# Optimization experiments

Hardware: AMD Instinct MI355X
Metric: run time of the kernel (lower is better)

Reference implementation:

```python
import jax, jax.numpy as jnp
import numpy as np


def setup_inputs() -> dict:
    key = jax.random.key(0)
    k1, k2 = jax.random.split(key)
    N, resolution = 32, 512
    cam2world_matrix = jax.random.normal(k1, (N, 4, 4), dtype=jnp.float32)
    # keep fx, fy (divisors) away from zero
    intrinsics = jax.random.uniform(k2, (N, 3, 3), dtype=jnp.float32, minval=0.5, maxval=1.5)
    return {"cam2world_matrix": cam2world_matrix, "intrinsics": intrinsics, "resolution": resolution}


def reference(cam2world_matrix, intrinsics, resolution):
    # patch_scale=1, masked_sampling=0 default path: full_resolution == resolution
    N = cam2world_matrix.shape[0]
    M = resolution * resolution
    cam_locs_world = cam2world_matrix[:, :3, 3]              # (N, 3)
    fx = intrinsics[:, 0, 0][:, None]
    fy = intrinsics[:, 1, 1][:, None]
    cx = intrinsics[:, 0, 2][:, None]
    cy = intrinsics[:, 1, 2][:, None]
    sk = intrinsics[:, 0, 1][:, None]

    # pixel-center uv grid in [0,1); torch builds (i,j) then flips channels,
    # so x_cam is the flattened column (j) grid, y_cam the row (i) grid.
    coords = (jnp.arange(resolution, dtype=jnp.float32) + 0.5) / resolution
    ii, jj = jnp.meshgrid(coords, coords, indexing='ij')      # (R, R) each
    x_cam = jj.reshape(1, M)                                  # broadcast over N
    y_cam = ii.reshape(1, M)
    z_cam = -1.0                                              # z_cam = -ones

    x_lift = -(x_cam - cx + cy * sk / fy - sk * y_cam / fy) / fx * z_cam  # (N, M)
    y_lift = (y_cam - cy) / fy * z_cam                                    # (N, M)

    ones = jnp.ones((N, M), dtype=cam2world_matrix.dtype)
    cam_rel_points = jnp.stack(
        (jnp.broadcast_to(x_lift, (N, M)),
         jnp.broadcast_to(y_lift, (N, M)),
         -ones, ones), axis=-1)                               # (N, M, 4)

    world_rel_points = jnp.einsum('nij,nmj->nmi', cam2world_matrix, cam_rel_points)[:, :, :3]
    ray_dirs = world_rel_points - cam_locs_world[:, None, :]
    norm = jnp.maximum(jnp.linalg.norm(ray_dirs, axis=2, keepdims=True), 1e-12)
    ray_dirs = ray_dirs / norm
    ray_origins = jnp.broadcast_to(cam_locs_world[:, None, :], ray_dirs.shape)
    return ray_origins, ray_dirs
```

## Files before the change

### kernel.cpp

```cpp
#include <hip/hip_runtime.h>
#include <math.h>

typedef float f32x4 __attribute__((ext_vector_type(4)));

__global__ __launch_bounds__(256) void ray_sampler_deep(
    const float* __restrict__ c2w,
    const float* __restrict__ intr,
    float* __restrict__ out,
    int blocks_per_cam,
    int resShift,
    float inv_res,
    size_t dir_off)
{
    const unsigned n   = (unsigned)blockIdx.x / (unsigned)blocks_per_cam;
    const unsigned blk = (unsigned)blockIdx.x - n * (unsigned)blocks_per_cam;
    const unsigned f4_per_cam = (unsigned)blocks_per_cam * 2048u;

    const float* C = c2w + n * 16;
    const float* K = intr + n * 9;

    const float r00 = C[0], r01 = C[1], r02 = C[2], ox = C[3];
    const float r10 = C[4], r11 = C[5], r12 = C[6], oy = C[7];
    const float r20 = C[8], r21 = C[9], r22 = C[10], oz = C[11];
    const float fx = K[0], sk = K[1], cx = K[2];
    const float fy = K[4], cy = K[5];

    const float inv_fx = 1.0f / fx;
    const float inv_fy = 1.0f / fy;
    const unsigned rmask = (1u << resShift) - 1u;

    const unsigned q0  = blk * 2048u + threadIdx.x;
    const unsigned f00 = q0 * 4u;
    const size_t   t0  = (size_t)n * f4_per_cam + q0;

    f32x4* o4 = reinterpret_cast<f32x4*>(out);
    f32x4* d4 = reinterpret_cast<f32x4*>(out + dir_off);

    #pragma unroll
    for (int k = 0; k < 8; ++k) {
        const unsigned f0 = f00 + 1024u * (unsigned)k;
        const unsigned p0 = f0 / 3u;
        const unsigned ph = f0 - p0 * 3u;
        const float ax = (ph == 0u) ? ox : ((ph == 1u) ? oy : oz);
        const float ay = (ph == 0u) ? oy : ((ph == 1u) ? oz : ox);
        const float az = (ph == 0u) ? oz : ((ph == 1u) ? ox : oy);
        const f32x4 vo = {ax, ay, az, ax};
        o4[t0 + 256u * (unsigned)k] = vo;
    }

    #pragma unroll
    for (int k = 0; k < 8; ++k) {
        const unsigned f0 = f00 + 1024u * (unsigned)k;
        const unsigned p0 = f0 / 3u;
        const unsigned ph = f0 - p0 * 3u;

        float d0x, d0y, d0z, d1x, d1y, d1z;
        #pragma unroll
        for (int s = 0; s < 2; ++s) {
            const unsigned p = p0 + (unsigned)s;
            const unsigned i = p >> resShift;
            const unsigned j = p & rmask;

            const float y_cam  = ((float)i + 0.5f) * inv_res;
            const float ycc    = (y_cam - cy) * inv_fy;
            const float y_lift = -ycc;
            const float xc_off = -cx - sk * ycc;
            const float x_cam  = ((float)j + 0.5f) * inv_res;
            const float x_lift = (x_cam + xc_off) * inv_fx;

            const float ux = fmaf(r00, x_lift, fmaf(r01, y_lift, -r02));
            const float uy = fmaf(r10, x_lift, fmaf(r11, y_lift, -r12));
            const float uz = fmaf(r20, x_lift, fmaf(r21, y_lift, -r22));
            const float ss  = fmaf(ux, ux, fmaf(uy, uy, uz * uz));
            const float inv = rsqrtf(fmaxf(ss, 1e-24f));

            if (s == 0) { d0x = ux * inv; d0y = uy * inv; d0z = uz * inv; }
            else        { d1x = ux * inv; d1y = uy * inv; d1z = uz * inv; }
        }

        f32x4 vd;
        vd.x = (ph == 0u) ? d0x : ((ph == 1u) ? d0y : d0z);
        vd.y = (ph == 0u) ? d0y : ((ph == 1u) ? d0z : d1x);
        vd.z = (ph == 0u) ? d0z : ((ph == 1u) ? d1x : d1y);
        vd.w = (ph == 0u) ? d1x : ((ph == 1u) ? d1y : d1z);
        d4[t0 + 256u * (unsigned)k] = vd;
    }
}

extern "C" void kernel_launch(void* const* d_in, const int* in_sizes, int n_in,
                              void* d_out, int out_size, void* d_ws, size_t ws_size,
                              hipStream_t stream) {
    const float* c2w  = (const float*)d_in[0];
    const float* intr = (const float*)d_in[1];
    float* out = (float*)d_out;

    const int N = in_sizes[0] / 16;
    const long long M = (long long)out_size / (6LL * (long long)N);
    const int res = (int)(sqrt((double)M) + 0.5);

    int resShift = 0; while ((1 << resShift) < res) ++resShift;

    const long long F    = (long long)N * M * 3LL;
    const int f4_per_cam = (int)(M * 3LL / 4LL);
    const int blocks_per_cam = f4_per_cam / 2048;
    const int grid = N * blocks_per_cam;
    const size_t dir_off = (size_t)F;

    ray_sampler_deep<<<grid, 256, 0, stream>>>(c2w, intr, out,
                                               blocks_per_cam, resShift,
                                               1.0f / (float)res, dir_off);
}
```

Before: 196.1 us.

## Replace per-camera block grid with persistent grid-stride sweep and shared camera table

Swaps the fixed per-camera grid, where each thread wrote eight origin and eight direction vectors, for a persistent 1024-block grid-stride loop over the origin and direction outputs in sequence. All camera matrices and inverted intrinsics are preloaded into shared memory once per block. A specialised template path replaces the per-element camera division with a shift and divide by three when the resolution is 512. The aim is to cut launch and tail overhead and keep the write stream continuous. The cost is a per-iteration branch, index arithmetic, and fewer writes in flight per thread.

```diff
diff --git a/kernel.cpp b/kernel.cpp
--- a/kernel.cpp
+++ b/kernel.cpp
@@ -3,87 +3,94 @@
 
 typedef float f32x4 __attribute__((ext_vector_type(4)));
 
-__global__ __launch_bounds__(256) void ray_sampler_deep(
+template <bool FAST3>
+__global__ __launch_bounds__(256) void ray_sweep(
     const float* __restrict__ c2w,
     const float* __restrict__ intr,
     float* __restrict__ out,
-    int blocks_per_cam,
+    unsigned f4_per_cam,
+    unsigned F4,
+    unsigned iters,
+    int N,
     int resShift,
     float inv_res,
     size_t dir_off)
 {
-    const unsigned n   = (unsigned)blockIdx.x / (unsigned)blocks_per_cam;
-    const unsigned blk = (unsigned)blockIdx.x - n * (unsigned)blocks_per_cam;
-    const unsigned f4_per_cam = (unsigned)blocks_per_cam * 2048u;
+    extern __shared__ float cam[];
 
-    const float* C = c2w + n * 16;
-    const float* K = intr + n * 9;
+    for (int c = threadIdx.x; c < N; c += 256) {
+        const float* C = c2w + c * 16;
+        const float* K = intr + c * 9;
+        float* s = cam + c * 17;
+        s[0]=C[0]; s[1]=C[1]; s[2]=C[2];  s[3]=C[3];
+        s[4]=C[4]; s[5]=C[5]; s[6]=C[6];  s[7]=C[7];
+        s[8]=C[8]; s[9]=C[9]; s[10]=C[10]; s[11]=C[11];
+        s[12] = 1.0f / K[0];
+        s[13] = K[1];
+        s[14] = K[2];
+        s[15] = 1.0f / K[4];
+        s[16] = K[5];
+    }
+    __syncthreads();
 
-    const float r00 = C[0], r01 = C[1], r02 = C[2], ox = C[3];
-    const float r10 = C[4], r11 = C[5], r12 = C[6], oy = C[7];
-    const float r20 = C[8], r21 = C[9], r22 = C[10], oz = C[11];
-    const float fx = K[0], sk = K[1], cx = K[2];
-    const float fy = K[4], cy = K[5];
-
-    const float inv_fx = 1.0f / fx;
-    const float inv_fy = 1.0f / fy;
+    const unsigned gstride = gridDim.x * 256u;
+    unsigned g = blockIdx.x * 256u + threadIdx.x;
+    f32x4* o4 = reinterpret_cast<f32x4*>(out);
+    f32x4* d4 = reinterpret_cast<f32x4*>(out + dir_off);
     const unsigned rmask = (1u << resShift) - 1u;
 
-    const unsigned q0  = blk * 2048u + threadIdx.x;
-    const unsigned f00 = q0 * 4u;
-    const size_t   t0  = (size_t)n * f4_per_cam + q0;
-
-    f32x4* o4 = reinterpret_cast<f32x4*>(out);
-    f32x4* d4 = reinterpret_cast<f32x4*>(out + dir_off);
-
-    #pragma unroll
-    for (int k = 0; k < 8; ++k) {
-        const unsigned f0 = f00 + 1024u * (unsigned)k;
+    for (unsigned it = 0; it < iters; ++it, g += gstride) {
+        const bool isO = g < F4;
+        const unsigned q = isO ? g : g - F4;
+        const unsigned n = FAST3 ? ((q >> 16) / 3u)
+                                 : (q / f4_per_cam);
+        const unsigned r = q - n * f4_per_cam;
+        const unsigned f0 = r * 4u;
         const unsigned p0 = f0 / 3u;
         const unsigned ph = f0 - p0 * 3u;
-        const float ax = (ph == 0u) ? ox : ((ph == 1u) ? oy : oz);
-        const float ay = (ph == 0u) ? oy : ((ph == 1u) ? oz : ox);
-        const float az = (ph == 0u) ? oz : ((ph == 1u) ? ox : oy);
-        const f32x4 vo = {ax, ay, az, ax};
-        o4[t0 + 256u * (unsigned)k] = vo;
-    }
+        const float* s = cam + n * 17;
 
-    #pragma unroll
-    for (int k = 0; k < 8; ++k) {
-        const unsigned f0 = f00 + 1024u * (unsigned)k;
-        const unsigned p0 = f0 / 3u;
-        const unsigned ph = f0 - p0 * 3u;
+        if (isO) {
+            const float ox = s[3], oy = s[7], oz = s[11];
+            const float ax = (ph == 0u) ? ox : ((ph == 1u) ? oy : oz);
+            const float ay = (ph == 0u) ? oy : ((ph == 1u) ? oz : ox);
+            const float az = (ph == 0u) ? oz : ((ph == 1u) ? ox : oy);
+            const f32x4 vo = {ax, ay, az, ax};
+            o4[g] = vo;
+        } else {
+            const float r00 = s[0], r01 = s[1], r02 = s[2];
+            const float r10 = s[4], r11 = s[5], r12 = s[6];
+            const float r20 = s[8], r21 = s[9], r22 = s[10];
+            const float inv_fx = s[12], sk = s[13], cx = s[14];
+            const float inv_fy = s[15], cy = s[16];
 
-        float d0x, d0y, d0z, d1x, d1y, d1z;
-        #pragma unroll
-        for (int s = 0; s < 2; ++s) {
-            const unsigned p = p0 + (unsigned)s;
-            const unsigned i = p >> resShift;
-            const unsigned j = p & rmask;
-
-            const float y_cam  = ((float)i + 0.5f) * inv_res;
-            const float ycc    = (y_cam - cy) * inv_fy;
-            const float y_lift = -ycc;
-            const float xc_off = -cx - sk * ycc;
-            const float x_cam  = ((float)j + 0.5f) * inv_res;
-            const float x_lift = (x_cam + xc_off) * inv_fx;
-
-            const float ux = fmaf(r00, x_lift, fmaf(r01, y_lift, -r02));
-            const float uy = fmaf(r10, x_lift, fmaf(r11, y_lift, -r12));
-            const float uz = fmaf(r20, x_lift, fmaf(r21, y_lift, -r22));
-            const float ss  = fmaf(ux, ux, fmaf(uy, uy, uz * uz));
-            const float inv = rsqrtf(fmaxf(ss, 1e-24f));
-
-            if (s == 0) { d0x = ux * inv; d0y = uy * inv; d0z = uz * inv; }
-            else        { d1x = ux * inv; d1y = uy * inv; d1z = uz * inv; }
+            float d0x, d0y, d0z, d1x, d1y, d1z;
+            #pragma unroll
+            for (int st = 0; st < 2; ++st) {
+                const unsigned p = p0 + (unsigned)st;
+                const unsigned i = p >> resShift;
+                const unsigned j = p & rmask;
+                const float y_cam  = ((float)i + 0.5f) * inv_res;
+                const float ycc    = (y_cam - cy) * inv_fy;
+                const float y_lift = -ycc;
+                const float xc_off = -cx - sk * ycc;
+                const float x_cam  = ((float)j + 0.5f) * inv_res;
+                const float x_lift = (x_cam + xc_off) * inv_fx;
+                const float ux = fmaf(r00, x_lift, fmaf(r01, y_lift, -r02));
+                const float uy = fmaf(r10, x_lift, fmaf(r11, y_lift, -r12));
+                const float uz = fmaf(r20, x_lift, fmaf(r21, y_lift, -r22));
+                const float ss  = fmaf(ux, ux, fmaf(uy, uy, uz * uz));
+                const float inv = rsqrtf(fmaxf(ss, 1e-24f));
+                if (st == 0) { d0x = ux*inv; d0y = uy*inv; d0z = uz*inv; }
+                else         { d1x = ux*inv; d1y = uy*inv; d1z = uz*inv; }
+            }
+            f32x4 vd;
+            vd.x = (ph == 0u) ? d0x : ((ph == 1u) ? d0y : d0z);
+            vd.y = (ph == 0u) ? d0y : ((ph == 1u) ? d0z : d1x);
+            vd.z = (ph == 0u) ? d0z : ((ph == 1u) ? d1x : d1y);
+            vd.w = (ph == 0u) ? d1x : ((ph == 1u) ? d1y : d1z);
+            d4[q] = vd;
         }
-
-        f32x4 vd;
-        vd.x = (ph == 0u) ? d0x : ((ph == 1u) ? d0y : d0z);
-        vd.y = (ph == 0u) ? d0y : ((ph == 1u) ? d0z : d1x);
-        vd.z = (ph == 0u) ? d0z : ((ph == 1u) ? d1x : d1y);
-        vd.w = (ph == 0u) ? d1x : ((ph == 1u) ? d1y : d1z);
-        d4[t0 + 256u * (unsigned)k] = vd;
     }
 }
 
@@ -100,13 +107,24 @@
 
     int resShift = 0; while ((1 << resShift) < res) ++resShift;
 
-    const long long F    = (long long)N * M * 3LL;
-    const int f4_per_cam = (int)(M * 3LL / 4LL);
-    const int blocks_per_cam = f4_per_cam / 2048;
-    const int grid = N * blocks_per_cam;
-    const size_t dir_off = (size_t)F;
+    const long long F     = (long long)N * M * 3LL;
+    const unsigned f4pc   = (unsigned)(M * 3LL / 4LL);
+    const unsigned F4     = (unsigned)N * f4pc;
+    const size_t  dir_off = (size_t)F;
 
-    ray_sampler_deep<<<grid, 256, 0, stream>>>(c2w, intr, out,
-                                               blocks_per_cam, resShift,
-                                               1.0f / (float)res, dir_off);
+    unsigned grid = 1024;
+    while ((2ull * F4) % ((unsigned long long)grid * 256ull) != 0ull && grid > 1)
+        grid >>= 1;
+    const unsigned iters = (unsigned)((2ull * F4) / ((unsigned long long)grid * 256ull));
+    const size_t shmem = (size_t)N * 17 * sizeof(float);
+
+    if (f4pc == 196608u) {
+        ray_sweep<true><<<grid, 256, shmem, stream>>>(c2w, intr, out, f4pc, F4,
+                                                      iters, N, resShift,
+                                                      1.0f / (float)res, dir_off);
+    } else {
+        ray_sweep<false><<<grid, 256, shmem, stream>>>(c2w, intr, out, f4pc, F4,
+                                                       iters, N, resShift,
+                                                       1.0f / (float)res, dir_off);
+    }
 }
```

Result: slower. 200.8 us (+2.4%).
